# Optimization experiments

Hardware: AMD Instinct MI355X
Metric: run time of the kernel (lower is better)

Reference implementation:

```python
import jax, jax.numpy as jnp
import numpy as np

C = 192
NUM_HEADS = 4
K = 3
KV_STRIDE = 2
EPS = 1e-5


def _conv(x, w, stride, groups):
    # x: [B,C,H,W], w: [O, I//groups, kh, kw]
    return jax.lax.conv_general_dilated(
        x, w, window_strides=(stride, stride),
        padding=[(K // 2, K // 2), (K // 2, K // 2)] if w.shape[-1] > 1 else [(0, 0), (0, 0)],
        dimension_numbers=("NCHW", "OIHW", "NCHW"),
        feature_group_count=groups)


def _bn(x, gamma, beta, mean, var):
    # eval-mode batchnorm over channel dim of NCHW
    inv = gamma / jnp.sqrt(var + EPS)
    return x * inv[None, :, None, None] + (beta - mean * inv)[None, :, None, None]


def _dwconv_flatten(x, dw, g, b, m, v, pw, stride):
    y = _conv(x, dw, stride, groups=C)          # depthwise
    y = _bn(y, g, b, m, v)
    y = _conv(y, pw, 1, groups=1)               # 1x1 pointwise
    B, O, h, w = y.shape
    return y.reshape(B, O, h * w).transpose(0, 2, 1)  # b (h w) c


def setup_inputs() -> dict:
    key = jax.random.key(0)
    ks = jax.random.split(key, 16)
    B, H, W = 8, 56, 56
    d = {
        "x": jax.random.normal(ks[0], (B, H * W, C), jnp.float32),
        "H": H,
        "W": W,
        "dw_q": jax.random.normal(ks[1], (C, 1, K, K), jnp.float32) * 0.1,
        "bn_q_gamma": jax.random.uniform(ks[2], (C,), jnp.float32, 0.5, 1.5),
        "bn_q_beta": jax.random.normal(ks[3], (C,), jnp.float32) * 0.1,
        "bn_q_mean": jax.random.normal(ks[4], (C,), jnp.float32) * 0.1,
        "bn_q_var": jax.random.uniform(ks[5], (C,), jnp.float32, 0.5, 1.5),
        "pw_q": jax.random.normal(ks[6], (C, C, 1, 1), jnp.float32) * (1.0 / np.sqrt(C)),
        "dw_kv": jax.random.normal(ks[7], (C, 1, K, K), jnp.float32) * 0.1,
        "bn_kv_gamma": jax.random.uniform(ks[8], (C,), jnp.float32, 0.5, 1.5),
        "bn_kv_beta": jax.random.normal(ks[9], (C,), jnp.float32) * 0.1,
        "bn_kv_mean": jax.random.normal(ks[10], (C,), jnp.float32) * 0.1,
        "bn_kv_var": jax.random.uniform(ks[11], (C,), jnp.float32, 0.5, 1.5),
        "pw_kv": jax.random.normal(ks[12], (2 * C, C, 1, 1), jnp.float32) * (1.0 / np.sqrt(C)),
        "Wq": jax.random.normal(ks[13], (C, C), jnp.float32) * (1.0 / np.sqrt(C)),
        "bq": jnp.zeros((C,), jnp.float32),
        "Wk": jax.random.normal(ks[14], (C, C), jnp.float32) * (1.0 / np.sqrt(C)),
        "bk": jnp.zeros((C,), jnp.float32),
        "Wv": jax.random.normal(ks[15], (C, C), jnp.float32) * (1.0 / np.sqrt(C)),
        "bv": jnp.zeros((C,), jnp.float32),
    }
    return d


def reference(x, H, W, dw_q, bn_q_gamma, bn_q_beta, bn_q_mean, bn_q_var, pw_q,
              dw_kv, bn_kv_gamma, bn_kv_beta, bn_kv_mean, bn_kv_var, pw_kv,
              Wq, bq, Wk, bk, Wv, bv):
    B, N, _ = x.shape
    h = NUM_HEADS
    hd = C // h
    scale = hd ** -0.5
    # Token2Patch: b (H W) c -> b c H W
    xp = x.transpose(0, 2, 1).reshape(B, C, H, W)
    conv_q = _dwconv_flatten(xp, dw_q, bn_q_gamma, bn_q_beta, bn_q_mean, bn_q_var, pw_q, 1)  # [B,N,C]
    kv = _dwconv_flatten(xp, dw_kv, bn_kv_gamma, bn_kv_beta, bn_kv_mean, bn_kv_var, pw_kv, KV_STRIDE)  # [B,M,2C]
    conv_k, conv_v = kv[..., :C], kv[..., C:]
    q = (conv_q @ Wq.T + bq).reshape(B, N, h, hd).transpose(0, 2, 1, 3)      # [B,h,N,hd]
    M = conv_k.shape[1]
    k = (conv_k @ Wk.T + bk).reshape(B, M, h, hd).transpose(0, 2, 1, 3)      # [B,h,M,hd]
    v = (conv_v @ Wv.T + bv).reshape(B, M, h, hd).transpose(0, 2, 1, 3)      # [B,h,M,hd]
    attn = jnp.einsum("bhnd,bhmd->bhnm", q, k) * scale
    attn = jax.nn.softmax(attn, axis=-1)
    out = jnp.einsum("bhnm,bhmd->bhnd", attn, v)
    # MergeHeads: b h n d -> b n (h d)
    return out.transpose(0, 2, 1, 3).reshape(B, N, C)
```

## Files before the change

kernel.cpp:

```cpp
#include <hip/hip_runtime.h>
#include <cmath>

typedef _Float16 f16;
typedef _Float16 f16x8 __attribute__((ext_vector_type(8)));
typedef _Float16 f16x4 __attribute__((ext_vector_type(4)));
typedef float    f32x4 __attribute__((ext_vector_type(4)));
typedef unsigned int u32;
typedef u32 u32x2 __attribute__((ext_vector_type(2)));

#define C_   192
#define HH   56
#define WW   56
#define NN   3136
#define BB   8
#define MM   784
#define NHEAD 4
#define HD   48
#define VT_LD 832
#define QPB  (BB*NN/64)
#define KVPB (BB*MM/64)

#define MFMA16(a,b,c)  __builtin_amdgcn_mfma_f32_16x16x32_f16(a,b,c,0,0,0)
#define MFMAK16(a,b,c) __builtin_amdgcn_mfma_f32_16x16x16f16(a,b,c,0,0,0)

static __device__ __forceinline__ u32 pkrtz(float a, float b) {
    typedef __fp16 fp16x2 __attribute__((ext_vector_type(2)));
    fp16x2 h = __builtin_amdgcn_cvt_pkrtz(a, b);
    return __builtin_bit_cast(u32, h);
}

static __device__ __forceinline__ void gload16(const void* g, void* l) {
    __builtin_amdgcn_global_load_lds(
        (const __attribute__((address_space(1))) unsigned int*)g,
        (__attribute__((address_space(3))) unsigned int*)l, 16, 0, 0);
}

template<int STRIDE, int OH, int OW>
__device__ __forceinline__ void dwbn_pair(
    const float* __restrict__ x, const float* __restrict__ dwL,
    const float* __restrict__ gamma, const float* __restrict__ beta,
    const float* __restrict__ mean,  const float* __restrict__ var,
    f16* __restrict__ out, int idx)
{
    int c4 = idx % 48;
    int r1 = idx / 48;
    int ox = r1 % OW;
    int r2 = r1 / OW;
    int p  = r2 % (OH/2);
    int b  = r2 / (OH/2);
    int c0 = c4*4;

    float4 w4[9];
    #pragma unroll
    for (int j = 0; j < 9; ++j)
        w4[j] = *(const float4*)&dwL[c4*40 + j*4];
    const float* wf = (const float*)w4;

    float4 g4  = *(const float4*)(gamma + c0);
    float4 be4 = *(const float4*)(beta + c0);
    float4 m4  = *(const float4*)(mean + c0);
    float4 v4  = *(const float4*)(var  + c0);

    const int NR = STRIDE + 3;
    float4 a0 = make_float4(0.f,0.f,0.f,0.f), a1 = a0;
    int iyTop = (2*p)*STRIDE - 1;
    int ix0 = ox*STRIDE - 1;
    #pragma unroll
    for (int j = 0; j < NR; ++j) {
        int iy = iyTop + j;
        if (iy < 0 || iy >= HH) continue;
        #pragma unroll
        for (int kx = 0; kx < 3; ++kx) {
            int ix = ix0 + kx;
            if (ix < 0 || ix >= WW) continue;
            float4 xv = *reinterpret_cast<const float4*>(
                x + ((size_t)b*NN + iy*WW + ix)*C_ + c0);
            if (j <= 2) {
                const int wi = j*3 + kx;
                a0.x = fmaf(wf[ 0+wi], xv.x, a0.x);
                a0.y = fmaf(wf[ 9+wi], xv.y, a0.y);
                a0.z = fmaf(wf[18+wi], xv.z, a0.z);
                a0.w = fmaf(wf[27+wi], xv.w, a0.w);
            }
            if (j >= STRIDE) {
                const int wi = (j-STRIDE)*3 + kx;
                a1.x = fmaf(wf[ 0+wi], xv.x, a1.x);
                a1.y = fmaf(wf[ 9+wi], xv.y, a1.y);
                a1.z = fmaf(wf[18+wi], xv.z, a1.z);
                a1.w = fmaf(wf[27+wi], xv.w, a1.w);
            }
        }
    }
    float i0 = g4.x*__frsqrt_rn(v4.x + 1e-5f);
    float i1 = g4.y*__frsqrt_rn(v4.y + 1e-5f);
    float i2 = g4.z*__frsqrt_rn(v4.z + 1e-5f);
    float i3 = g4.w*__frsqrt_rn(v4.w + 1e-5f);
    float b0 = be4.x - m4.x*i0, b1 = be4.y - m4.y*i1;
    float b2 = be4.z - m4.z*i2, b3 = be4.w - m4.w*i3;
    f16x4 r0, r1v;
    r0[0] = (f16)(a0.x*i0 + b0); r0[1] = (f16)(a0.y*i1 + b1);
    r0[2] = (f16)(a0.z*i2 + b2); r0[3] = (f16)(a0.w*i3 + b3);
    r1v[0] = (f16)(a1.x*i0 + b0); r1v[1] = (f16)(a1.y*i1 + b1);
    r1v[2] = (f16)(a1.z*i2 + b2); r1v[3] = (f16)(a1.w*i3 + b3);
    size_t o0 = (((size_t)b*OH + 2*p)*OW + ox)*48 + c4;
    *reinterpret_cast<f16x4*>(out + o0*4)            = r0;
    *reinterpret_cast<f16x4*>(out + (o0 + (size_t)OW*48)*4) = r1v;
}

__global__ __launch_bounds__(256) void prep_all(
    const float* __restrict__ x,
    const float* __restrict__ dwq,  const float* __restrict__ gq,
    const float* __restrict__ bq_,  const float* __restrict__ mq,
    const float* __restrict__ vq,
    const float* __restrict__ dwkv, const float* __restrict__ gkv,
    const float* __restrict__ bkv,  const float* __restrict__ mkv,
    const float* __restrict__ vkv,
    const float* __restrict__ Wq, const float* __restrict__ Wk,
    const float* __restrict__ Wv, const float* __restrict__ pw_q,
    const float* __restrict__ pw_kv,
    f16* __restrict__ uq, f16* __restrict__ ukv,
    f16* __restrict__ Mq, f16* __restrict__ Mk, f16* __restrict__ Mv,
    f16* __restrict__ vt)
{
    int blk = blockIdx.x, tid = threadIdx.x;
    const int QB = 2352, KB = 588;
    if (blk < QB + KB) {
        bool qp = blk < QB;
        __shared__ __align__(16) float dwL[48*40];
        const float* dwg = qp ? dwq : dwkv;
        for (int i = tid; i < 432; i += 256) {
            int f  = i*4;
            int c4 = f/36, r = f%36;
            *(float4*)&dwL[c4*40 + r] = *(const float4*)(dwg + f);
        }
        __syncthreads();
        if (qp)
            dwbn_pair<1, HH, WW>(x, dwL, gq, bq_, mq, vq, uq, blk*256 + tid);
        else
            dwbn_pair<2, 28, 28>(x, dwL, gkv, bkv, mkv, vkv, ukv,
                                 (blk - QB)*256 + tid);
    } else if (blk < QB + KB + 576) {
        int fb = blk - QB - KB;
        int which = fb / 192, o = fb % 192;
        const float* Wm = which == 0 ? Wq : (which == 1 ? Wk : Wv);
        const float* P  = which == 0 ? pw_q : (which == 1 ? pw_kv : pw_kv + C_*C_);
        f16* Mo         = which == 0 ? Mq : (which == 1 ? Mk : Mv);
        __shared__ float wrow[C_];
        if (tid < C_) wrow[tid] = Wm[o*C_ + tid];
        __syncthreads();
        if (tid < C_) {
            float acc = 0.f;
            #pragma unroll 8
            for (int j = 0; j < C_; ++j)
                acc = fmaf(wrow[j], P[j*C_ + tid], acc);
            Mo[o*C_ + tid] = (f16)acc;
        }
    } else {
        int i = (blk - QB - KB - 576)*256 + tid;
        int b = i / (C_*48);
        int rem = i % (C_*48);
        int c = rem / 48;
        int m = MM + (rem % 48);
        vt[((size_t)b*C_ + c)*VT_LD + m] = (f16)0.f;
    }
}

__global__ __launch_bounds__(256, 1) void proj_all(
    const f16* __restrict__ uq, const f16* __restrict__ ukv,
    const f16* __restrict__ Mq, const f16* __restrict__ Mk,
    const f16* __restrict__ Mv,
    const float* __restrict__ bq, const float* __restrict__ bk,
    const float* __restrict__ bv,
    f16* __restrict__ qb, f16* __restrict__ kb, f16* __restrict__ vt)
{
    int tid  = threadIdx.x;
    int w    = tid >> 6, l = tid & 63;
    int lrow = l & 15,  lgrp = l >> 4;
    int blk  = blockIdx.x;
    int path = blk < QPB ? 0 : (blk < QPB + KVPB ? 1 : 2);
    const f16* U = path == 0 ? uq : ukv;
    int rblk = path == 0 ? blk : (path == 1 ? blk - QPB : blk - QPB - KVPB);
    int r0 = rblk*64 + w*16;

    const f16* urow = U + (size_t)(r0 + lrow)*C_;
    f16x8 a[6];
    #pragma unroll
    for (int ch = 0; ch < 6; ++ch)
        a[ch] = *(const f16x8*)(urow + ch*32 + lgrp*8);

    f16x8 bfA[6], bfB[6];
    const f16* Mm = path == 0 ? Mq : (path == 1 ? Mk : Mv);

    #pragma unroll
    for (int ch = 0; ch < 6; ++ch)
        bfA[ch] = *(const f16x8*)(Mm + (size_t)lrow*C_ + ch*32 + lgrp*8);

    if (path < 2) {
        const float sc = path == 0 ? 0.14433756729740643f*1.4426950408889634f
                                   : 1.0f;
        const float* bias = path == 0 ? bq : bk;
        f16* dst = path == 0 ? qb : kb;
        #pragma unroll
        for (int ct = 0; ct < 12; ++ct) {
            f16x8* cur = (ct & 1) ? bfB : bfA;
            f16x8* nxt = (ct & 1) ? bfA : bfB;
            if (ct < 11) {
                const f16* mrow = Mm + (size_t)((ct+1)*16 + lrow)*C_;
                #pragma unroll
                for (int ch = 0; ch < 6; ++ch)
                    nxt[ch] = *(const f16x8*)(mrow + ch*32 + lgrp*8);
            }
            f32x4 acc = {0.f,0.f,0.f,0.f};
            #pragma unroll
            for (int ch = 0; ch < 6; ++ch)
                acc = MFMA16(cur[ch], a[ch], acc);
            float4 bo = *(const float4*)(bias + ct*16 + lgrp*4);
            f16x4 st;
            st[0] = (f16)((acc[0] + bo.x)*sc);
            st[1] = (f16)((acc[1] + bo.y)*sc);
            st[2] = (f16)((acc[2] + bo.z)*sc);
            st[3] = (f16)((acc[3] + bo.w)*sc);
            *(f16x4*)(dst + (size_t)(r0 + lrow)*C_ + ct*16 + lgrp*4) = st;
        }
    } else {
        #pragma unroll
        for (int ct = 0; ct < 12; ++ct) {
            f16x8* cur = (ct & 1) ? bfB : bfA;
            f16x8* nxt = (ct & 1) ? bfA : bfB;
            if (ct < 11) {
                const f16* mrow = Mv + (size_t)((ct+1)*16 + lrow)*C_;
                #pragma unroll
                for (int ch = 0; ch < 6; ++ch)
                    nxt[ch] = *(const f16x8*)(mrow + ch*32 + lgrp*8);
            }
            int o = ct*16 + lrow;
            f32x4 acc = {0.f,0.f,0.f,0.f};
            #pragma unroll
            for (int ch = 0; ch < 6; ++ch)
                acc = MFMA16(a[ch], cur[ch], acc);
            float bo = bv[o];
            int rg = r0 + lgrp*4;
            int b  = rg / MM, m = rg % MM;
            f16x4 st;
            st[0] = (f16)(acc[0] + bo);
            st[1] = (f16)(acc[1] + bo);
            st[2] = (f16)(acc[2] + bo);
            st[3] = (f16)(acc[3] + bo);
            *(f16x4*)(vt + ((size_t)b*C_ + o)*VT_LD + m) = st;
        }
    }
}

__device__ __forceinline__ void stage_tile(
    int w, int l, f16* ldsKb, f16* ldsVb,
    const f16* __restrict__ kbb, const f16* __restrict__ vbb, int m0)
{
    int rr = l >> 3, p = l & 7;
    #pragma unroll
    for (int j = 0; j < 4; ++j) {
        int u = w + j*4;
        if (u < 8) {
            int r = u*8 + rr;
            int c = p ^ (r & 7);
            gload16(kbb + (size_t)(m0 + r)*C_ + c*8, ldsKb + u*512);
        } else if (u < 14) {
            int d = (u-8)*8 + rr;
            int c = p ^ (d & 7);
            gload16(vbb + (size_t)d*VT_LD + m0 + c*8, ldsVb + (u-8)*512);
        }
    }
}

__device__ __forceinline__ float softmax_upd(
    f32x4* s, float& mrun, float& lrun, u32* pk)
{
    float t0 = fmaxf(fmaxf(s[0][0], s[0][1]), fmaxf(s[0][2], s[0][3]));
    float t1 = fmaxf(fmaxf(s[1][0], s[1][1]), fmaxf(s[1][2], s[1][3]));
    float t2 = fmaxf(fmaxf(s[2][0], s[2][1]), fmaxf(s[2][2], s[2][3]));
    float t3 = fmaxf(fmaxf(s[3][0], s[3][1]), fmaxf(s[3][2], s[3][3]));
    float tmax = fmaxf(fmaxf(t0, t1), fmaxf(t2, t3));
    tmax = fmaxf(tmax, __shfl_xor(tmax, 16));
    tmax = fmaxf(tmax, __shfl_xor(tmax, 32));
    float mnew = fmaxf(mrun, tmax);
    float corr = exp2f(mrun - mnew);
    mrun = mnew;
    float psum = 0.f;
    #pragma unroll
    for (int j = 0; j < 4; ++j) {
        #pragma unroll
        for (int r = 0; r < 4; ++r) {
            s[j][r] = exp2f(s[j][r] - mnew);
            psum += s[j][r];
        }
    }
    lrun = lrun*corr + psum;
    #pragma unroll
    for (int j = 0; j < 4; ++j) {
        pk[j*2]   = pkrtz(s[j][0], s[j][1]);
        pk[j*2+1] = pkrtz(s[j][2], s[j][3]);
    }
    return corr;
}

__device__ __forceinline__ void compute_tile64(
    const f16* ldsKb, const f16* ldsVb,
    const f16x8& qf0, const f16x4& qfh,
    float& mrun, float& lrun, f32x4& o0, f32x4& o1, f32x4& o2,
    int lrow, int g, bool tail)
{
    const char* kP = (const char*)ldsKb;
    const char* vP = (const char*)ldsVb;
    f32x4 z = {0.f,0.f,0.f,0.f};
    int sw = lrow & 7;
    int cA = (g ^ sw) << 4;
    int cH = (((4 + (g >> 1)) ^ sw) << 4) + ((g & 1) << 3);

    f32x4 s[4];
    __builtin_amdgcn_s_setprio(1);
    #pragma unroll
    for (int j = 0; j < 4; ++j) {
        const char* rb = kP + (16*j + lrow)*128;
        f32x4 t = MFMA16(*(const f16x8*)(rb + cA), qf0, z);
        s[j] = MFMAK16(*(const f16x4*)(rb + cH), qfh, t);
    }
    __builtin_amdgcn_s_setprio(0);

    if (tail) {
        f32x4 neg = {-1e30f,-1e30f,-1e30f,-1e30f};
        s[1] = neg; s[2] = neg; s[3] = neg;
    }

    u32 pk[8];
    float corr = softmax_upd(s, mrun, lrun, pk);

    #pragma unroll
    for (int r = 0; r < 4; ++r) { o0[r] *= corr; o1[r] *= corr; o2[r] *= corr; }

    #pragma unroll
    for (int ch = 0; ch < 4; ++ch) {
        u32x2 pw = { pk[2*ch], pk[2*ch+1] };
        f16x4 pb = __builtin_bit_cast(f16x4, pw);
        int off = (((2*ch + (g >> 1)) ^ sw) << 4) + ((g & 1) << 3);
        f16x4 v0 = *(const f16x4*)(vP + lrow*128      + off);
        f16x4 v1 = *(const f16x4*)(vP + (16+lrow)*128 + off);
        f16x4 v2 = *(const f16x4*)(vP + (32+lrow)*128 + off);
        __builtin_amdgcn_s_setprio(1);
        o0 = MFMAK16(v0, pb, o0);
        o1 = MFMAK16(v1, pb, o1);
        o2 = MFMAK16(v2, pb, o2);
        __builtin_amdgcn_s_setprio(0);
    }
}

__global__ __launch_bounds__(256, 4) void attn_mfma(
    const f16* __restrict__ qb, const f16* __restrict__ kb,
    const f16* __restrict__ vt, float* __restrict__ out)
{
    __shared__ __align__(16) f16 ldsK[2][64*64];
    __shared__ __align__(16) f16 ldsV[2][48*64];

    int tid  = threadIdx.x;
    int w    = tid >> 6, l = tid & 63;
    int lrow = l & 15,  g = l >> 4;
    int swz  = (blockIdx.x & 7)*196 + (blockIdx.x >> 3);
    int bh   = swz / 49, qblk = swz % 49;
    int h    = bh & 3, b = bh >> 2;
    int n0   = qblk*64 + w*16;

    const f16* kbb = kb + (size_t)b*MM*C_ + h*HD;
    const f16* vbb = vt + ((size_t)b*C_ + h*HD)*VT_LD;

    const f16* qrow = qb + ((size_t)b*NN + n0 + lrow)*C_ + h*HD;
    f16x8 qf0 = *(const f16x8*)(qrow + g*8);
    f16x4 qfh = *(const f16x4*)(qrow + 32 + g*4);
    asm volatile("" :: "v"(qf0), "v"(qfh));

    float mrun = -1e30f, lrun = 0.f;
    f32x4 o0 = {0.f,0.f,0.f,0.f}, o1 = o0, o2 = o0;

    stage_tile(w, l, &ldsK[0][0], &ldsV[0][0], kbb, vbb, 0);

    for (int t = 0; t < 13; ++t) {
        int nb = t & 1;
        if (t < 12)
            stage_tile(w, l, &ldsK[nb^1][0], &ldsV[nb^1][0], kbb, vbb, (t+1)*64);
        __builtin_amdgcn_sched_barrier(0);
        if (t < 12) {
            if (w < 2) asm volatile("s_waitcnt vmcnt(4)" ::: "memory");
            else       asm volatile("s_waitcnt vmcnt(3)" ::: "memory");
        } else {
            asm volatile("s_waitcnt vmcnt(0)" ::: "memory");
        }
        __builtin_amdgcn_s_barrier();
        __builtin_amdgcn_sched_barrier(0);
        compute_tile64(&ldsK[nb][0], &ldsV[nb][0], qf0, qfh,
                       mrun, lrun, o0, o1, o2, lrow, g, t == 12);
        __builtin_amdgcn_sched_barrier(0);
        __builtin_amdgcn_s_barrier();
    }

    lrun += __shfl_xor(lrun, 16);
    lrun += __shfl_xor(lrun, 32);
    float inv = 1.f / lrun;
    f32x4 r0, r1, r2;
    #pragma unroll
    for (int r = 0; r < 4; ++r) {
        r0[r] = o0[r]*inv; r1[r] = o1[r]*inv; r2[r] = o2[r]*inv;
    }
    float* obase = out + ((size_t)b*NN + n0 + lrow)*C_ + h*HD + g*4;
    *(f32x4*)(obase)      = r0;
    *(f32x4*)(obase + 16) = r1;
    *(f32x4*)(obase + 32) = r2;
}

extern "C" void kernel_launch(void* const* d_in, const int* in_sizes, int n_in,
                              void* d_out, int out_size, void* d_ws, size_t ws_size,
                              hipStream_t stream)
{
    const float* x     = (const float*)d_in[0];
    const float* dw_q  = (const float*)d_in[3];
    const float* bnqg  = (const float*)d_in[4];
    const float* bnqb  = (const float*)d_in[5];
    const float* bnqm  = (const float*)d_in[6];
    const float* bnqv  = (const float*)d_in[7];
    const float* pw_q  = (const float*)d_in[8];
    const float* dw_kv = (const float*)d_in[9];
    const float* bnkg  = (const float*)d_in[10];
    const float* bnkb  = (const float*)d_in[11];
    const float* bnkm  = (const float*)d_in[12];
    const float* bnkvv = (const float*)d_in[13];
    const float* pw_kv = (const float*)d_in[14];
    const float* Wq    = (const float*)d_in[15];
    const float* bq    = (const float*)d_in[16];
    const float* Wk    = (const float*)d_in[17];
    const float* bk    = (const float*)d_in[18];
    const float* Wv    = (const float*)d_in[19];
    const float* bv    = (const float*)d_in[20];
    float* out = (float*)d_out;

    f16* p   = (f16*)d_ws;
    f16* Mq16  = p;  p += C_*C_;
    f16* Mk16  = p;  p += C_*C_;
    f16* Mv16  = p;  p += C_*C_;
    f16* uq16  = p;  p += (size_t)BB*NN*C_;
    f16* ukv16 = p;  p += (size_t)BB*MM*C_;
    f16* qb16  = p;  p += (size_t)BB*NN*C_ + 256;
    f16* kb16  = p;  p += (size_t)BB*MM*C_ + 16384;
    f16* vt16  = p;  p += (size_t)BB*C_*VT_LD;

    prep_all<<<3804, 256, 0, stream>>>(
        x, dw_q, bnqg, bnqb, bnqm, bnqv,
        dw_kv, bnkg, bnkb, bnkm, bnkvv,
        Wq, Wk, Wv, pw_q, pw_kv,
        uq16, ukv16, Mq16, Mk16, Mv16, vt16);

    proj_all<<<QPB + 2*KVPB, 256, 0, stream>>>(
        uq16, ukv16, Mq16, Mk16, Mv16, bq, bk, bv, qb16, kb16, vt16);

    attn_mfma<<<1568, 256, 0, stream>>>(qb16, kb16, vt16, out);
}
```

Before: 108.1 us.

## Compute 2x2 output quads in depthwise conv and halve projection block size

The depthwise conv+BN prep now has each thread produce a 2x2 patch of outputs instead of a vertical pair, so overlapping input pixels are loaded once and reused across four accumulators. The prep grid shrinks to match. Separately, the projection kernel drops from 4 to 2 waves per block, handling 32 rows per block and launching twice as many blocks. This trades more registers per thread in the conv for fewer redundant global loads, and gives the projection finer-grained parallelism. Any code in the unseen part of proj_all that still assumes four waves or 64 rows would be wrong.

```diff
diff --git a/kernel.cpp b/kernel.cpp
--- a/kernel.cpp
+++ b/kernel.cpp
@@ -17,8 +17,8 @@
 #define NHEAD 4
 #define HD   48
 #define VT_LD 832
-#define QPB  (BB*NN/64)
-#define KVPB (BB*MM/64)
+#define QPB  (BB*NN/32)
+#define KVPB (BB*MM/32)
 
 #define MFMA16(a,b,c)  __builtin_amdgcn_mfma_f32_16x16x32_f16(a,b,c,0,0,0)
 #define MFMAK16(a,b,c) __builtin_amdgcn_mfma_f32_16x16x16f16(a,b,c,0,0,0)
@@ -36,7 +36,7 @@
 }
 
 template<int STRIDE, int OH, int OW>
-__device__ __forceinline__ void dwbn_pair(
+__device__ __forceinline__ void dwbn_quad(
     const float* __restrict__ x, const float* __restrict__ dwL,
     const float* __restrict__ gamma, const float* __restrict__ beta,
     const float* __restrict__ mean,  const float* __restrict__ var,
@@ -44,9 +44,9 @@
 {
     int c4 = idx % 48;
     int r1 = idx / 48;
-    int ox = r1 % OW;
-    int r2 = r1 / OW;
-    int p  = r2 % (OH/2);
+    int qx = r1 % (OW/2);
+    int r2 = r1 / (OW/2);
+    int qp = r2 % (OH/2);
     int b  = r2 / (OH/2);
     int c0 = c4*4;
 
@@ -61,34 +61,42 @@
     float4 m4  = *(const float4*)(mean + c0);
     float4 v4  = *(const float4*)(var  + c0);
 
-    const int NR = STRIDE + 3;
-    float4 a0 = make_float4(0.f,0.f,0.f,0.f), a1 = a0;
-    int iyTop = (2*p)*STRIDE - 1;
-    int ix0 = ox*STRIDE - 1;
-    #pragma unroll
-    for (int j = 0; j < NR; ++j) {
+    float4 a00 = make_float4(0.f,0.f,0.f,0.f);
+    float4 a01 = a00, a10 = a00, a11 = a00;
+    int iyTop = (2*qp)*STRIDE - 1;
+    int ix0   = (2*qx)*STRIDE - 1;
+    #pragma unroll
+    for (int j = 0; j < STRIDE+3; ++j) {
         int iy = iyTop + j;
         if (iy < 0 || iy >= HH) continue;
         #pragma unroll
-        for (int kx = 0; kx < 3; ++kx) {
-            int ix = ix0 + kx;
+        for (int i = 0; i < STRIDE+3; ++i) {
+            int ix = ix0 + i;
             if (ix < 0 || ix >= WW) continue;
             float4 xv = *reinterpret_cast<const float4*>(
                 x + ((size_t)b*NN + iy*WW + ix)*C_ + c0);
-            if (j <= 2) {
-                const int wi = j*3 + kx;
-                a0.x = fmaf(wf[ 0+wi], xv.x, a0.x);
-                a0.y = fmaf(wf[ 9+wi], xv.y, a0.y);
-                a0.z = fmaf(wf[18+wi], xv.z, a0.z);
-                a0.w = fmaf(wf[27+wi], xv.w, a0.w);
-            }
-            if (j >= STRIDE) {
-                const int wi = (j-STRIDE)*3 + kx;
-                a1.x = fmaf(wf[ 0+wi], xv.x, a1.x);
-                a1.y = fmaf(wf[ 9+wi], xv.y, a1.y);
-                a1.z = fmaf(wf[18+wi], xv.z, a1.z);
-                a1.w = fmaf(wf[27+wi], xv.w, a1.w);
-            }
+            const bool r0ok = (j <= 2), r1ok = (j >= STRIDE);
+            const bool c0ok = (i <= 2), c1ok = (i >= STRIDE);
+            if (r0ok && c0ok) { const int wi = j*3 + i;
+                a00.x = fmaf(wf[ 0+wi], xv.x, a00.x);
+                a00.y = fmaf(wf[ 9+wi], xv.y, a00.y);
+                a00.z = fmaf(wf[18+wi], xv.z, a00.z);
+                a00.w = fmaf(wf[27+wi], xv.w, a00.w); }
+            if (r0ok && c1ok) { const int wi = j*3 + (i-STRIDE);
+                a01.x = fmaf(wf[ 0+wi], xv.x, a01.x);
+                a01.y = fmaf(wf[ 9+wi], xv.y, a01.y);
+                a01.z = fmaf(wf[18+wi], xv.z, a01.z);
+                a01.w = fmaf(wf[27+wi], xv.w, a01.w); }
+            if (r1ok && c0ok) { const int wi = (j-STRIDE)*3 + i;
+                a10.x = fmaf(wf[ 0+wi], xv.x, a10.x);
+                a10.y = fmaf(wf[ 9+wi], xv.y, a10.y);
+                a10.z = fmaf(wf[18+wi], xv.z, a10.z);
+                a10.w = fmaf(wf[27+wi], xv.w, a10.w); }
+            if (r1ok && c1ok) { const int wi = (j-STRIDE)*3 + (i-STRIDE);
+                a11.x = fmaf(wf[ 0+wi], xv.x, a11.x);
+                a11.y = fmaf(wf[ 9+wi], xv.y, a11.y);
+                a11.z = fmaf(wf[18+wi], xv.z, a11.z);
+                a11.w = fmaf(wf[27+wi], xv.w, a11.w); }
         }
     }
     float i0 = g4.x*__frsqrt_rn(v4.x + 1e-5f);
@@ -97,14 +105,20 @@
     float i3 = g4.w*__frsqrt_rn(v4.w + 1e-5f);
     float b0 = be4.x - m4.x*i0, b1 = be4.y - m4.y*i1;
     float b2 = be4.z - m4.z*i2, b3 = be4.w - m4.w*i3;
-    f16x4 r0, r1v;
-    r0[0] = (f16)(a0.x*i0 + b0); r0[1] = (f16)(a0.y*i1 + b1);
-    r0[2] = (f16)(a0.z*i2 + b2); r0[3] = (f16)(a0.w*i3 + b3);
-    r1v[0] = (f16)(a1.x*i0 + b0); r1v[1] = (f16)(a1.y*i1 + b1);
-    r1v[2] = (f16)(a1.z*i2 + b2); r1v[3] = (f16)(a1.w*i3 + b3);
-    size_t o0 = (((size_t)b*OH + 2*p)*OW + ox)*48 + c4;
-    *reinterpret_cast<f16x4*>(out + o0*4)            = r0;
-    *reinterpret_cast<f16x4*>(out + (o0 + (size_t)OW*48)*4) = r1v;
+    size_t base = (((size_t)b*OH + 2*qp)*OW + 2*qx)*48 + c4;
+    f16x4 r;
+    r[0]=(f16)(a00.x*i0+b0); r[1]=(f16)(a00.y*i1+b1);
+    r[2]=(f16)(a00.z*i2+b2); r[3]=(f16)(a00.w*i3+b3);
+    *reinterpret_cast<f16x4*>(out + base*4) = r;
+    r[0]=(f16)(a01.x*i0+b0); r[1]=(f16)(a01.y*i1+b1);
+    r[2]=(f16)(a01.z*i2+b2); r[3]=(f16)(a01.w*i3+b3);
+    *reinterpret_cast<f16x4*>(out + (base + 48)*4) = r;
+    r[0]=(f16)(a10.x*i0+b0); r[1]=(f16)(a10.y*i1+b1);
+    r[2]=(f16)(a10.z*i2+b2); r[3]=(f16)(a10.w*i3+b3);
+    *reinterpret_cast<f16x4*>(out + (base + (size_t)OW*48)*4) = r;
+    r[0]=(f16)(a11.x*i0+b0); r[1]=(f16)(a11.y*i1+b1);
+    r[2]=(f16)(a11.z*i2+b2); r[3]=(f16)(a11.w*i3+b3);
+    *reinterpret_cast<f16x4*>(out + (base + (size_t)OW*48 + 48)*4) = r;
 }
 
 __global__ __launch_bounds__(256) void prep_all(
@@ -123,7 +137,7 @@
     f16* __restrict__ vt)
 {
     int blk = blockIdx.x, tid = threadIdx.x;
-    const int QB = 2352, KB = 588;
+    const int QB = 1176, KB = 294;
     if (blk < QB + KB) {
         bool qp = blk < QB;
         __shared__ __align__(16) float dwL[48*40];
@@ -135,9 +149,9 @@
         }
         __syncthreads();
         if (qp)
-            dwbn_pair<1, HH, WW>(x, dwL, gq, bq_, mq, vq, uq, blk*256 + tid);
+            dwbn_quad<1, HH, WW>(x, dwL, gq, bq_, mq, vq, uq, blk*256 + tid);
         else
-            dwbn_pair<2, 28, 28>(x, dwL, gkv, bkv, mkv, vkv, ukv,
+            dwbn_quad<2, 28, 28>(x, dwL, gkv, bkv, mkv, vkv, ukv,
                                  (blk - QB)*256 + tid);
     } else if (blk < QB + KB + 576) {
         int fb = blk - QB - KB;
@@ -165,7 +179,7 @@
     }
 }
 
-__global__ __launch_bounds__(256, 1) void proj_all(
+__global__ __launch_bounds__(128, 1) void proj_all(
     const f16* __restrict__ uq, const f16* __restrict__ ukv,
     const f16* __restrict__ Mq, const f16* __restrict__ Mk,
     const f16* __restrict__ Mv,
@@ -180,7 +194,7 @@
     int path = blk < QPB ? 0 : (blk < QPB + KVPB ? 1 : 2);
     const f16* U = path == 0 ? uq : ukv;
     int rblk = path == 0 ? blk : (path == 1 ? blk - QPB : blk - QPB - KVPB);
-    int r0 = rblk*64 + w*16;
+    int r0 = rblk*32 + w*16;
 
     const f16* urow = U + (size_t)(r0 + lrow)*C_;
     f16x8 a[6];
@@ -448,13 +462,13 @@
     f16* kb16  = p;  p += (size_t)BB*MM*C_ + 16384;
     f16* vt16  = p;  p += (size_t)BB*C_*VT_LD;
 
-    prep_all<<<3804, 256, 0, stream>>>(
+    prep_all<<<2334, 256, 0, stream>>>(
         x, dw_q, bnqg, bnqb, bnqm, bnqv,
         dw_kv, bnkg, bnkb, bnkm, bnkvv,
         Wq, Wk, Wv, pw_q, pw_kv,
         uq16, ukv16, Mq16, Mk16, Mv16, vt16);
 
-    proj_all<<<QPB + 2*KVPB, 256, 0, stream>>>(
+    proj_all<<<QPB + 2*KVPB, 128, 0, stream>>>(
         uq16, ukv16, Mq16, Mk16, Mv16, bq, bk, bv, qb16, kb16, vt16);
 
     attn_mfma<<<1568, 256, 0, stream>>>(qb16, kb16, vt16, out);
```

After: 104.3 us. 3.6% less time.
